# Kernel tuning notes

Measured on AMD Instinct MI355X. Metric: run time of the kernel, lower is better.

The kernel has to match this reference:

```python
import jax, jax.numpy as jnp
import numpy as np

B, S, D = 2, 2048, 1024
H = 16
HD = D // H


def setup_inputs() -> dict:
    key = jax.random.key(0)
    ks = jax.random.split(key, 6)
    X = jax.random.normal(ks[0], (B, S, D), dtype=jnp.float32)
    # Linear weights stored [in, out] so y = x @ W (torch stores transposed).
    sc = 1.0 / np.sqrt(D)
    Wq = jax.random.normal(ks[1], (D, D), dtype=jnp.float32) * sc
    Wk = jax.random.normal(ks[2], (D, D), dtype=jnp.float32) * sc
    Wv = jax.random.normal(ks[3], (D, D), dtype=jnp.float32) * sc
    Wo = jax.random.normal(ks[4], (D, D), dtype=jnp.float32) * sc
    bo = jax.random.normal(ks[5], (D,), dtype=jnp.float32) * 0.01
    return {"X": X, "Wq": Wq, "Wk": Wk, "Wv": Wv, "Wo": Wo, "bo": bo}


def reference(X, Wq, Wk, Wv, Wo, bo):
    b, n, _ = X.shape
    # QKV projections (no bias, qkv_bias=False), reshape to [b, h, n, hd]
    q = (X @ Wq).reshape(b, n, H, HD).transpose(0, 2, 1, 3)
    k = (X @ Wk).reshape(b, n, H, HD).transpose(0, 2, 1, 3)
    v = (X @ Wv).reshape(b, n, H, HD).transpose(0, 2, 1, 3)
    # Unscaled scores (module's scale flag defaults to False)
    scores = jnp.einsum("bhqd,bhkd->bhqk", q, k)
    causal = jnp.triu(jnp.ones((n, n), dtype=bool), k=1)  # True above diagonal
    scores = jnp.where(causal, -jnp.inf, scores)
    attn = jax.nn.softmax(scores, axis=-1)
    # dropout p=0.0 -> identity
    ctx = jnp.einsum("bhqk,bhkd->bqhd", attn, v).reshape(b, n, H * HD)
    return ctx @ Wo + bo
```

## Files before the change

### kernel.cpp

```cpp
#include <hip/hip_runtime.h>
#include <stdint.h>


typedef __attribute__((ext_vector_type(8))) short short8;
typedef __attribute__((ext_vector_type(4))) float floatx4;

#define S_LEN 2048
#define D_DIM 1024
#define NH 16
#define HD 64
#define L2E 1.44269504088896340736f

__device__ __forceinline__ short f2bf(float f) {
    uint32_t u = __builtin_bit_cast(uint32_t, f);
    uint32_t r = u + 0x7fffu + ((u >> 16) & 1u);
    return (short)(r >> 16);
}
__device__ __forceinline__ uint32_t pack2(float a, float b) {
#if __has_builtin(__builtin_amdgcn_cvt_pk_bf16_f32)
    auto v = __builtin_amdgcn_cvt_pk_bf16_f32(a, b);
    uint32_t r; __builtin_memcpy(&r, &v, sizeof(r)); return r;
#else
    return (uint32_t)(uint16_t)f2bf(a) | ((uint32_t)(uint16_t)f2bf(b) << 16);
#endif
}
__device__ __forceinline__ void gll16(const void* g, void* l) {
    __builtin_amdgcn_global_load_lds(
        (const __attribute__((address_space(1))) void*)g,
        (__attribute__((address_space(3))) void*)l, 16, 0, 0);
}

__global__ __launch_bounds__(256) void castx_kernel(const float* __restrict__ X,
                                                    short* __restrict__ Xb) {
    int i = blockIdx.x * 256 + threadIdx.x;
    const float4 v = *(const float4*)(X + (size_t)i * 4);
    uint2 o;
    o.x = pack2(v.x, v.y);
    o.y = pack2(v.z, v.w);
    *(uint2*)(Xb + (size_t)i * 4) = o;
}

__global__ __launch_bounds__(256) void tcast4_kernel(const float* __restrict__ Wq,
                                                     const float* __restrict__ Wk,
                                                     const float* __restrict__ Wv,
                                                     const float* __restrict__ Wo,
                                                     short* __restrict__ WqkvT,
                                                     short* __restrict__ WoT) {
    const int z = blockIdx.z;
    const float* W = (z == 0) ? Wq : (z == 1) ? Wk : (z == 2) ? Wv : Wo;
    short* WT = (z < 3) ? (WqkvT + (size_t)z * 1024 * 1024) : WoT;
    __shared__ float tile[32][33];
    const int bx = blockIdx.x * 32;
    const int by = blockIdx.y * 32;
    const int tx = threadIdx.x, ty = threadIdx.y;
    for (int i = 0; i < 32; i += 8)
        tile[ty + i][tx] = W[(size_t)(bx + ty + i) * D_DIM + by + tx];
    __syncthreads();
    for (int i = 0; i < 32; i += 8)
        WT[(size_t)(by + ty + i) * D_DIM + bx + tx] = f2bf(tile[tx][ty + i]);
}

__device__ __forceinline__ void gemm_main8(const short* __restrict__ A,
                                           const short* __restrict__ BT,
                                           short* As, short* Bs,
                                           int m0, int n0, floatx4 (&acc)[4][2],
                                           int tid) {
    const int lane = tid & 63, ln = lane & 15, quad = lane >> 4;
    const int wave = tid >> 6;
    const int mw = (wave & 1) * 64, nw = (wave >> 1) * 32;
    for (int k0 = 0; k0 < D_DIM; k0 += 64) {
        __syncthreads();
        for (int t = 0; t < 2; t++) {
            const int c = t * 512 + tid;
            const int row = c >> 3, pos = c & 7, src = pos ^ (row & 7);
            gll16(A  + (size_t)(m0 + row) * D_DIM + k0 + src * 8, As + c * 8);
            gll16(BT + (size_t)(n0 + row) * D_DIM + k0 + src * 8, Bs + c * 8);
        }
        __syncthreads();
        for (int ks = 0; ks < 2; ks++) {
            short8 a[4], b[2];
            for (int i = 0; i < 4; i++) {
                const int row = mw + i * 16 + ln;
                a[i] = *(const short8*)(As + row * 64 + (((ks * 4 + quad) ^ (ln & 7)) * 8));
            }
            for (int j = 0; j < 2; j++) {
                const int row = nw + j * 16 + ln;
                b[j] = *(const short8*)(Bs + row * 64 + (((ks * 4 + quad) ^ (ln & 7)) * 8));
            }
            for (int i = 0; i < 4; i++)
                for (int j = 0; j < 2; j++)
                    acc[i][j] = __builtin_amdgcn_mfma_f32_16x16x32_bf16(a[i], b[j], acc[i][j], 0, 0, 0);
        }
    }
}

__global__ __launch_bounds__(512) void gemm_qkv_kernel(const short* __restrict__ Xb,
                                                       const short* __restrict__ WT,
                                                       short* __restrict__ Qb,
                                                       short* __restrict__ Kb,
                                                       short* __restrict__ Vtb) {
    __shared__ __align__(16) short As[128 * 64];
    __shared__ __align__(16) short Bs[128 * 64];
    const int m0 = blockIdx.x * 128, n0 = blockIdx.y * 128;
    floatx4 acc[4][2] = {};
    gemm_main8(Xb, WT, As, Bs, m0, n0, acc, threadIdx.x);

    const int tid = threadIdx.x, wave = tid >> 6, lane = tid & 63;
    const int ln = lane & 15, quad = lane >> 4;
    const int mw = (wave & 1) * 64, nw = (wave >> 1) * 32;
    const int nsel = n0 >> 10;
    const float qs = (nsel == 0) ? L2E : 1.f;
    short* outB = (nsel == 0) ? Qb : (nsel == 1 ? Kb : Vtb);
    for (int i = 0; i < 4; i++)
        for (int j = 0; j < 2; j++)
            for (int r = 0; r < 4; r++) {
                const int row = m0 + mw + i * 16 + quad * 4 + r;
                const int col = (n0 & 1023) + nw + j * 16 + ln;
                const int bb = row >> 11, s = row & (S_LEN - 1);
                const int h = col >> 6, hd = col & (HD - 1);
                const short v = f2bf(acc[i][j][r] * qs);
                if (nsel < 2)
                    outB[(((size_t)(bb * NH + h)) * S_LEN + s) * HD + hd] = v;
                else
                    outB[(((size_t)(bb * NH + h)) * HD + hd) * S_LEN + s] = v;
            }
}

__global__ __launch_bounds__(512) void gemm_out_kernel(const short* __restrict__ Cb,
                                                       const short* __restrict__ WoT,
                                                       float* __restrict__ out,
                                                       const float* __restrict__ bias) {
    __shared__ __align__(16) short As[128 * 64];
    __shared__ __align__(16) short Bs[64 * 64];
    const int m0 = blockIdx.x * 128, n0 = blockIdx.y * 64;
    const int tid = threadIdx.x, lane = tid & 63;
    const int ln = lane & 15, quad = lane >> 4;
    const int wave = tid >> 6;
    const int mw = (wave & 3) * 32, nw = (wave >> 2) * 32;

    floatx4 acc[2][2] = {};

    for (int k0 = 0; k0 < D_DIM; k0 += 64) {
        __syncthreads();
        for (int t = 0; t < 2; t++) {
            const int c = t * 512 + tid;
            const int row = c >> 3, pos = c & 7, src = pos ^ (row & 7);
            gll16(Cb + (size_t)(m0 + row) * D_DIM + k0 + src * 8, As + c * 8);
        }
        {
            const int c = tid;
            const int row = c >> 3, pos = c & 7, src = pos ^ (row & 7);
            gll16(WoT + (size_t)(n0 + row) * D_DIM + k0 + src * 8, Bs + c * 8);
        }
        __syncthreads();
        for (int ks = 0; ks < 2; ks++) {
            short8 a[2], b[2];
            for (int i = 0; i < 2; i++) {
                const int row = mw + i * 16 + ln;
                a[i] = *(const short8*)(As + row * 64 + (((ks * 4 + quad) ^ (ln & 7)) * 8));
            }
            for (int j = 0; j < 2; j++) {
                const int row = nw + j * 16 + ln;
                b[j] = *(const short8*)(Bs + row * 64 + (((ks * 4 + quad) ^ (ln & 7)) * 8));
            }
            for (int i = 0; i < 2; i++)
                for (int j = 0; j < 2; j++)
                    acc[i][j] = __builtin_amdgcn_mfma_f32_16x16x32_bf16(a[i], b[j], acc[i][j], 0, 0, 0);
        }
    }

    for (int i = 0; i < 2; i++)
        for (int j = 0; j < 2; j++)
            for (int r = 0; r < 4; r++) {
                const int row = m0 + mw + i * 16 + quad * 4 + r;
                const int col = n0 + nw + j * 16 + ln;
                out[(size_t)row * D_DIM + col] = acc[i][j][r] + bias[col];
            }
}

#define PST 136

__global__ __launch_bounds__(256, 3) void attn_kernel(const short* __restrict__ Q,
                                                      const short* __restrict__ Kg,
                                                      const short* __restrict__ Vt,
                                                      short* __restrict__ ctx,
                                                      float* __restrict__ Opart,
                                                      float* __restrict__ Lpart) {
    __shared__ __align__(16) short Ks[128 * 64];
    __shared__ __align__(16) short Vs[64 * 128];
    __shared__ __align__(16) short Ps[4][16 * PST];

    const int tid = threadIdx.x, wave = tid >> 6, lane = tid & 63;
    const int ln = lane & 15, quad = lane >> 4;

    const int id = blockIdx.x;
    const int bh = (id & 7) + 8 * ((id >> 3) & 3);
    const int t = id >> 5;
    int qt, k_begin, k_end, pidx;
    if (t < 32) {
        qt = 31 - (t >> 1);
        const int half = t & 1;
        const int n = (qt + 2) >> 1;
        const int h0 = n >> 1;
        k_begin = half ? h0 : 0;
        k_end   = half ? n  : h0;
        pidx = ((qt - 16) * 32 + bh) * 2 + half;
    } else {
        qt = 47 - t;
        k_begin = 0; k_end = (qt + 2) >> 1;
        pidx = -1;
    }
    const int kmask = ((qt + 2) >> 1) - 1;
    const int q0 = qt * 64;
    const int bb = bh >> 4, h = bh & 15;
    short* Pw = &Ps[wave][0];

    const short* qrow = Q + ((size_t)bh * S_LEN + q0 + wave * 16 + ln) * HD;
    const short8 qb0 = *(const short8*)(qrow + quad * 8);
    const short8 qb1 = *(const short8*)(qrow + 32 + quad * 8);
    const int q_abs = q0 + wave * 16 + ln;

    float l_part = 0.f;
    floatx4 o_acc[4] = {};

    for (int kt = k_begin; kt < k_end; kt++) {
        const int k0 = kt * 128;
        __syncthreads();
        for (int tt = 0; tt < 4; tt++) {
            const int c = tt * 256 + tid;
            {
                const int row = c >> 3, pos = c & 7, src = pos ^ (row & 7);
                gll16(Kg + ((size_t)bh * S_LEN + k0 + row) * HD + src * 8, Ks + c * 8);
            }
            {
                const int row = c >> 4, pos = c & 15, src = pos ^ (row & 15);
                gll16(Vt + ((size_t)bh * HD + row) * S_LEN + k0 + src * 8, Vs + c * 8);
            }
        }
        __syncthreads();

        floatx4 sc[8];
        for (int nt = 0; nt < 8; nt++) {
            const int row = nt * 16 + ln;
            const short8 ak0 = *(const short8*)(Ks + row * 64 + ((quad ^ (ln & 7)) * 8));
            const short8 ak1 = *(const short8*)(Ks + row * 64 + (((4 + quad) ^ (ln & 7)) * 8));
            floatx4 z = {};
            z = __builtin_amdgcn_mfma_f32_16x16x32_bf16(ak0, qb0, z, 0, 0, 0);
            z = __builtin_amdgcn_mfma_f32_16x16x32_bf16(ak1, qb1, z, 0, 0, 0);
            sc[nt] = z;
        }

        if (kt == kmask) {
            for (int nt = 0; nt < 8; nt++)
                for (int r = 0; r < 4; r++)
                    if (k0 + nt * 16 + quad * 4 + r > q_abs) sc[nt][r] = -1e30f;
        }

        float ls = 0.f;
        for (int nt = 0; nt < 8; nt++)
            for (int r = 0; r < 4; r++) {
                const float e = exp2f(sc[nt][r]);
                sc[nt][r] = e; ls += e;
            }
        l_part += ls;

        for (int nt = 0; nt < 8; nt++) {
            uint2 u;
            u.x = pack2(sc[nt][0], sc[nt][1]);
            u.y = pack2(sc[nt][2], sc[nt][3]);
            *(uint2*)&Pw[ln * PST + nt * 16 + quad * 4] = u;
        }

        for (int ks = 0; ks < 4; ks++) {
            const short8 bp = *(const short8*)&Pw[ln * PST + ks * 32 + quad * 8];
            for (int dt = 0; dt < 4; dt++) {
                const int row = dt * 16 + ln;
                const short8 av = *(const short8*)(Vs + row * 128 + (((ks * 4 + quad) ^ (ln & 15)) * 8));
                o_acc[dt] = __builtin_amdgcn_mfma_f32_16x16x32_bf16(av, bp, o_acc[dt], 0, 0, 0);
            }
        }
    }

    float l_tot = l_part;
    l_tot += __shfl_xor(l_tot, 16, 64);
    l_tot += __shfl_xor(l_tot, 32, 64);

    if (pidx >= 0) {
        float* Ob = Opart + (size_t)pidx * 4096 + (wave * 16 + ln) * 64;
        for (int dt = 0; dt < 4; dt++)
            *(float4*)(Ob + dt * 16 + quad * 4) = *(float4*)&o_acc[dt];
        if (quad == 0) Lpart[(size_t)pidx * 64 + wave * 16 + ln] = l_tot;
    } else {
        const float rl = 1.f / l_tot;
        for (int dt = 0; dt < 4; dt++) {
            uint2 u;
            u.x = pack2(o_acc[dt][0] * rl, o_acc[dt][1] * rl);
            u.y = pack2(o_acc[dt][2] * rl, o_acc[dt][3] * rl);
            *(uint2*)&Pw[ln * PST + dt * 16 + quad * 4] = u;
        }
        const int qr = lane >> 2, sg = lane & 3;
        for (int c = 0; c < 2; c++) {
            const short8 v = *(const short8*)&Pw[qr * PST + sg * 8 + c * 32];
            const int s = q0 + wave * 16 + qr;
            *(short8*)(ctx + ((size_t)bb * S_LEN + s) * D_DIM + h * HD + sg * 8 + c * 32) = v;
        }
    }
}

__global__ __launch_bounds__(256) void combine_kernel(const float* __restrict__ Opart,
                                                      const float* __restrict__ Lpart,
                                                      short* __restrict__ ctx) {
    const int tile = blockIdx.x;
    const int qt = 16 + (tile >> 5), bh = tile & 31;
    const int bb = bh >> 4, h = bh & 15;
    const int p0 = ((qt - 16) * 32 + bh) * 2;
    const float* O0 = Opart + (size_t)p0 * 4096;
    const float* O1 = O0 + 4096;
    const float* l0 = Lpart + (size_t)p0 * 64;
    const float* l1 = l0 + 64;
    for (int e = threadIdx.x; e < 1024; e += 256) {
        const int q = e >> 4, seg = e & 15;
        const float rl = 1.f / (l0[q] + l1[q]);
        const float4 x0 = *(const float4*)(O0 + q * 64 + seg * 4);
        const float4 x1 = *(const float4*)(O1 + q * 64 + seg * 4);
        uint2 u;
        u.x = pack2((x0.x + x1.x) * rl, (x0.y + x1.y) * rl);
        u.y = pack2((x0.z + x1.z) * rl, (x0.w + x1.w) * rl);
        const int s = qt * 64 + q;
        *(uint2*)(ctx + ((size_t)bb * S_LEN + s) * D_DIM + h * HD + seg * 4) = u;
    }
}

extern "C" void kernel_launch(void* const* d_in, const int* in_sizes, int n_in,
                              void* d_out, int out_size, void* d_ws, size_t ws_size,
                              hipStream_t stream) {
    const float* X  = (const float*)d_in[0];
    const float* Wq = (const float*)d_in[1];
    const float* Wk = (const float*)d_in[2];
    const float* Wv = (const float*)d_in[3];
    const float* Wo = (const float*)d_in[4];
    const float* bo = (const float*)d_in[5];
    float* out = (float*)d_out;

    char* ws = (char*)d_ws;
    const size_t MB = 1024 * 1024;
    short* Xb     = (short*)(ws);
    short* WqkvT  = (short*)(ws + 8  * MB);
    short* Qb     = (short*)(ws + 16 * MB);
    short* Kb     = (short*)(ws + 24 * MB);
    short* Vtb    = (short*)(ws + 32 * MB);
    short* ctxb   = (short*)(ws + 40 * MB);
    short* WoT    = (short*)(ws + 48 * MB);
    float* Opart  = (float*)(ws);
    float* Lpart  = (float*)(ws + 50 * MB);

    castx_kernel<<<4096, 256, 0, stream>>>(X, Xb);
    dim3 tg(32, 32, 4), tb(32, 8);
    tcast4_kernel<<<tg, tb, 0, stream>>>(Wq, Wk, Wv, Wo, WqkvT, WoT);

    dim3 gq(32, 24);
    gemm_qkv_kernel<<<gq, 512, 0, stream>>>(Xb, WqkvT, Qb, Kb, Vtb);

    attn_kernel<<<1536, 256, 0, stream>>>(Qb, Kb, Vtb, ctxb, Opart, Lpart);
    combine_kernel<<<512, 256, 0, stream>>>(Opart, Lpart, ctxb);

    dim3 go(32, 16);
    gemm_out_kernel<<<go, 512, 0, stream>>>(ctxb, WoT, out, bo);
}
```

Measured before the change: 182.0 us.

## Use 128-row query tiles with 8 waves and a static task schedule

Attention blocks now cover 128 query rows with 512 threads (8 waves), so each K/V tile loaded into LDS serves twice as many queries. A hand-written 24-entry task table assigns query tiles and split-K halves to balance causal work, and the combine kernel is updated to match. The P staging buffer becomes a smaller double-buffered chunk per pair of score tiles, interleaved with the PV MFMAs, and s_setprio hints are added around the MFMA sections. Larger blocks may reduce occupancy and make the balance of the fixed schedule harder to verify.

Result: slower. 188.5 us (+3.5%).

```diff
diff --git a/kernel.cpp b/kernel.cpp
--- a/kernel.cpp
+++ b/kernel.cpp
@@ -178,9 +178,7 @@
             }
 }
 
-#define PST 136
-
-__global__ __launch_bounds__(256, 3) void attn_kernel(const short* __restrict__ Q,
+__global__ __launch_bounds__(512, 4) void attn_kernel(const short* __restrict__ Q,
                                                       const short* __restrict__ Kg,
                                                       const short* __restrict__ Vt,
                                                       short* __restrict__ ctx,
@@ -188,7 +186,7 @@
                                                       float* __restrict__ Lpart) {
     __shared__ __align__(16) short Ks[128 * 64];
     __shared__ __align__(16) short Vs[64 * 128];
-    __shared__ __align__(16) short Ps[4][16 * PST];
+    __shared__ __align__(16) short Ps[8][1280];
 
     const int tid = threadIdx.x, wave = tid >> 6, lane = tid & 63;
     const int ln = lane & 15, quad = lane >> 4;
@@ -196,24 +194,21 @@
     const int id = blockIdx.x;
     const int bh = (id & 7) + 8 * ((id >> 3) & 3);
     const int t = id >> 5;
-    int qt, k_begin, k_end, pidx;
-    if (t < 32) {
-        qt = 31 - (t >> 1);
-        const int half = t & 1;
-        const int n = (qt + 2) >> 1;
-        const int h0 = n >> 1;
-        k_begin = half ? h0 : 0;
-        k_end   = half ? n  : h0;
-        pidx = ((qt - 16) * 32 + bh) * 2 + half;
-    } else {
-        qt = 47 - t;
-        k_begin = 0; k_end = (qt + 2) >> 1;
-        pidx = -1;
-    }
-    const int kmask = ((qt + 2) >> 1) - 1;
-    const int q0 = qt * 64;
+
+    static const unsigned char TASK[24] = {
+        0xF0, 0x02, 0xF1, 0x12, 0xE1, 0x22, 0x72, 0x80,
+        0xE0, 0x32, 0xD0, 0xA0, 0xD1, 0x90, 0xC1, 0x91,
+        0xC0, 0x81, 0xB0, 0x42, 0xB1, 0xA1, 0x62, 0x52};
+    const int code = TASK[t];
+    const int qt = code >> 4, mode = code & 3;
+    const int n = qt + 1, h0 = n >> 1;
+    const int k_begin = (mode == 1) ? h0 : 0;
+    const int k_end   = (mode == 0) ? h0 : n;
+    const int pidx    = (mode == 2) ? -1 : ((qt - 8) * 32 + bh) * 2 + mode;
+    const int kmask = qt;
+    const int q0 = qt * 128;
     const int bb = bh >> 4, h = bh & 15;
-    short* Pw = &Ps[wave][0];
+    short* Pw = Ps[wave];
 
     const short* qrow = Q + ((size_t)bh * S_LEN + q0 + wave * 16 + ln) * HD;
     const short8 qb0 = *(const short8*)(qrow + quad * 8);
@@ -226,8 +221,8 @@
     for (int kt = k_begin; kt < k_end; kt++) {
         const int k0 = kt * 128;
         __syncthreads();
-        for (int tt = 0; tt < 4; tt++) {
-            const int c = tt * 256 + tid;
+        for (int tt = 0; tt < 2; tt++) {
+            const int c = tt * 512 + tid;
             {
                 const int row = c >> 3, pos = c & 7, src = pos ^ (row & 7);
                 gll16(Kg + ((size_t)bh * S_LEN + k0 + row) * HD + src * 8, Ks + c * 8);
@@ -240,6 +235,7 @@
         __syncthreads();
 
         floatx4 sc[8];
+        __builtin_amdgcn_s_setprio(1);
         for (int nt = 0; nt < 8; nt++) {
             const int row = nt * 16 + ln;
             const short8 ak0 = *(const short8*)(Ks + row * 64 + ((quad ^ (ln & 7)) * 8));
@@ -249,6 +245,7 @@
             z = __builtin_amdgcn_mfma_f32_16x16x32_bf16(ak1, qb1, z, 0, 0, 0);
             sc[nt] = z;
         }
+        __builtin_amdgcn_s_setprio(0);
 
         if (kt == kmask) {
             for (int nt = 0; nt < 8; nt++)
@@ -264,20 +261,23 @@
             }
         l_part += ls;
 
-        for (int nt = 0; nt < 8; nt++) {
-            uint2 u;
-            u.x = pack2(sc[nt][0], sc[nt][1]);
-            u.y = pack2(sc[nt][2], sc[nt][3]);
-            *(uint2*)&Pw[ln * PST + nt * 16 + quad * 4] = u;
-        }
-
-        for (int ks = 0; ks < 4; ks++) {
-            const short8 bp = *(const short8*)&Pw[ln * PST + ks * 32 + quad * 8];
+        for (int p = 0; p < 4; p++) {
+            short* Pq = Pw + (p & 1) * 640;
+            uint2 u0, u1;
+            u0.x = pack2(sc[2 * p][0], sc[2 * p][1]);
+            u0.y = pack2(sc[2 * p][2], sc[2 * p][3]);
+            u1.x = pack2(sc[2 * p + 1][0], sc[2 * p + 1][1]);
+            u1.y = pack2(sc[2 * p + 1][2], sc[2 * p + 1][3]);
+            *(uint2*)&Pq[ln * 40 + quad * 4]      = u0;
+            *(uint2*)&Pq[ln * 40 + 16 + quad * 4] = u1;
+            const short8 bp = *(const short8*)&Pq[ln * 40 + quad * 8];
+            __builtin_amdgcn_s_setprio(1);
             for (int dt = 0; dt < 4; dt++) {
                 const int row = dt * 16 + ln;
-                const short8 av = *(const short8*)(Vs + row * 128 + (((ks * 4 + quad) ^ (ln & 15)) * 8));
+                const short8 av = *(const short8*)(Vs + row * 128 + (((p * 4 + quad) ^ (ln & 15)) * 8));
                 o_acc[dt] = __builtin_amdgcn_mfma_f32_16x16x32_bf16(av, bp, o_acc[dt], 0, 0, 0);
             }
+            __builtin_amdgcn_s_setprio(0);
         }
     }
 
@@ -286,21 +286,21 @@
     l_tot += __shfl_xor(l_tot, 32, 64);
 
     if (pidx >= 0) {
-        float* Ob = Opart + (size_t)pidx * 4096 + (wave * 16 + ln) * 64;
+        float* Ob = Opart + (size_t)pidx * 8192 + (wave * 16 + ln) * 64;
         for (int dt = 0; dt < 4; dt++)
             *(float4*)(Ob + dt * 16 + quad * 4) = *(float4*)&o_acc[dt];
-        if (quad == 0) Lpart[(size_t)pidx * 64 + wave * 16 + ln] = l_tot;
+        if (quad == 0) Lpart[(size_t)pidx * 128 + wave * 16 + ln] = l_tot;
     } else {
         const float rl = 1.f / l_tot;
         for (int dt = 0; dt < 4; dt++) {
             uint2 u;
             u.x = pack2(o_acc[dt][0] * rl, o_acc[dt][1] * rl);
             u.y = pack2(o_acc[dt][2] * rl, o_acc[dt][3] * rl);
-            *(uint2*)&Pw[ln * PST + dt * 16 + quad * 4] = u;
+            *(uint2*)&Pw[(dt >> 1) * 640 + ln * 40 + (dt & 1) * 16 + quad * 4] = u;
         }
         const int qr = lane >> 2, sg = lane & 3;
         for (int c = 0; c < 2; c++) {
-            const short8 v = *(const short8*)&Pw[qr * PST + sg * 8 + c * 32];
+            const short8 v = *(const short8*)&Pw[c * 640 + qr * 40 + sg * 8];
             const int s = q0 + wave * 16 + qr;
             *(short8*)(ctx + ((size_t)bb * S_LEN + s) * D_DIM + h * HD + sg * 8 + c * 32) = v;
         }
@@ -311,14 +311,14 @@
                                                       const float* __restrict__ Lpart,
                                                       short* __restrict__ ctx) {
     const int tile = blockIdx.x;
-    const int qt = 16 + (tile >> 5), bh = tile & 31;
+    const int qt = 8 + (tile >> 5), bh = tile & 31;
     const int bb = bh >> 4, h = bh & 15;
-    const int p0 = ((qt - 16) * 32 + bh) * 2;
-    const float* O0 = Opart + (size_t)p0 * 4096;
-    const float* O1 = O0 + 4096;
-    const float* l0 = Lpart + (size_t)p0 * 64;
-    const float* l1 = l0 + 64;
-    for (int e = threadIdx.x; e < 1024; e += 256) {
+    const int p0 = ((qt - 8) * 32 + bh) * 2;
+    const float* O0 = Opart + (size_t)p0 * 8192;
+    const float* O1 = O0 + 8192;
+    const float* l0 = Lpart + (size_t)p0 * 128;
+    const float* l1 = l0 + 128;
+    for (int e = threadIdx.x; e < 2048; e += 256) {
         const int q = e >> 4, seg = e & 15;
         const float rl = 1.f / (l0[q] + l1[q]);
         const float4 x0 = *(const float4*)(O0 + q * 64 + seg * 4);
@@ -326,7 +326,7 @@
         uint2 u;
         u.x = pack2((x0.x + x1.x) * rl, (x0.y + x1.y) * rl);
         u.y = pack2((x0.z + x1.z) * rl, (x0.w + x1.w) * rl);
-        const int s = qt * 64 + q;
+        const int s = qt * 128 + q;
         *(uint2*)(ctx + ((size_t)bb * S_LEN + s) * D_DIM + h * HD + seg * 4) = u;
     }
 }
@@ -361,8 +361,8 @@
     dim3 gq(32, 24);
     gemm_qkv_kernel<<<gq, 512, 0, stream>>>(Xb, WqkvT, Qb, Kb, Vtb);
 
-    attn_kernel<<<1536, 256, 0, stream>>>(Qb, Kb, Vtb, ctxb, Opart, Lpart);
-    combine_kernel<<<512, 256, 0, stream>>>(Opart, Lpart, ctxb);
+    attn_kernel<<<768, 512, 0, stream>>>(Qb, Kb, Vtb, ctxb, Opart, Lpart);
+    combine_kernel<<<256, 256, 0, stream>>>(Opart, Lpart, ctxb);
 
     dim3 go(32, 16);
     gemm_out_kernel<<<go, 512, 0, stream>>>(ctxb, WoT, out, bo);
```
